# Performance work log

Measured on AMD Instinct MI355X. Metric: run time of the kernel, lower is better.

Reference implementation:

```python
import jax, jax.numpy as jnp
import numpy as np

B, L, H = 256, 16, 512
D2 = 2 * H  # bidirectional tree-LSTM hidden dim


def setup_inputs() -> dict:
    key = jax.random.key(0)
    ks = jax.random.split(key, 8)
    sc = lambda k, shp, fan: (jax.random.normal(k, shp, jnp.float32) / np.sqrt(fan)).astype(jnp.float32)
    return {
        "idiom_hidden": jax.random.normal(ks[0], (B, L, H), jnp.float32),
        "idiom_length": jax.random.randint(ks[1], (B,), 2, L + 1, jnp.int32),
        "w_ih_f": sc(ks[2], (4 * H, H), H),
        "w_hh_f": sc(ks[3], (4 * H, H), H),
        "b_f": jnp.zeros((4 * H,), jnp.float32),   # b_ih + b_hh fused
        "w_ih_b": sc(ks[4], (4 * H, H), H),
        "w_hh_b": sc(ks[5], (4 * H, H), H),
        "b_b": jnp.zeros((4 * H,), jnp.float32),
        "w_comp": sc(ks[6], (5 * D2, 2 * D2), 2 * D2),
        "b_comp": jnp.zeros((5 * D2,), jnp.float32),
        "w_query": sc(ks[7], (1, D2), D2),
    }


def _lstm(x, w_ih, w_hh, b):
    # x: (B, T, H) -> hs, cs: (B, T, H). PyTorch LSTMCell gate order: i, f, g, o.
    xg = jnp.einsum("bth,gh->btg", x, w_ih) + b  # precompute input gates

    def step(carry, xg_t):
        h, c = carry
        g = xg_t + h @ w_hh.T
        i, f, u, o = jnp.split(g, 4, axis=-1)
        c = jax.nn.sigmoid(f) * c + jax.nn.sigmoid(i) * jnp.tanh(u)
        h = jax.nn.sigmoid(o) * jnp.tanh(c)
        return (h, c), (h, c)

    z = jnp.zeros((x.shape[0], w_hh.shape[1]), x.dtype)
    _, (hs, cs) = jax.lax.scan(step, (z, z), jnp.swapaxes(xg, 0, 1))
    return jnp.swapaxes(hs, 0, 1), jnp.swapaxes(cs, 0, 1)


def _reverse_padded(x, lengths):
    # reverse first `length` positions of each sequence (batch_first)
    T = x.shape[1]
    pos = jnp.arange(T)[None, :]
    ln = lengths[:, None]
    idx = jnp.where(pos < ln, ln - 1 - pos, pos)
    return jnp.take_along_axis(x, idx[:, :, None], axis=1)


def _treelstm(hl, cl, hr, cr, w, b):
    v = jnp.concatenate([hl, hr], axis=-1) @ w.T + b
    i, fl, fr, u, o = jnp.split(v, 5, axis=-1)
    c = cl * jax.nn.sigmoid(fl + 1.0) + cr * jax.nn.sigmoid(fr + 1.0) + jnp.tanh(u) * jax.nn.sigmoid(i)
    h = jax.nn.sigmoid(o) * jnp.tanh(c)
    return h, c


def reference(idiom_hidden, idiom_length, w_ih_f, w_hh_f, b_f, w_ih_b, w_hh_b, b_b, w_comp, b_comp, w_query):
    maxd = idiom_hidden.shape[1]
    lmask = (jnp.arange(maxd)[None, :] < idiom_length[:, None]).astype(idiom_hidden.dtype)

    # bidirectional leaf LSTM
    hs_f, cs_f = _lstm(idiom_hidden, w_ih_f, w_hh_f, b_f)
    x_bw = _reverse_padded(idiom_hidden, idiom_length)
    hs_b, cs_b = _lstm(x_bw, w_ih_b, w_hh_b, b_b)
    hs_b = _reverse_padded(hs_b, idiom_length)
    cs_b = _reverse_padded(cs_b, idiom_length)
    h = jnp.concatenate([hs_f, hs_b], axis=-1)  # (B, L, 2H)
    c = jnp.concatenate([cs_f, cs_b], axis=-1)

    # iterative tree-LSTM composition (shapes shrink by 1 each step -> Python loop over depth)
    for i in range(maxd - 1):
        hl, hr = h[:, :-1, :], h[:, 1:, :]
        cl, cr = c[:, :-1, :], c[:, 1:, :]
        nh, nc = _treelstm(hl, cl, hr, cr, w_comp, b_comp)
        if i < maxd - 2:
            logits = jnp.einsum("bmd,d->bm", nh, w_query[0])
            m = lmask[:, i + 1:]
            masked = logits + (1.0 - m) * -10000.0  # eval-mode greedy_select
            sel = jax.lax.stop_gradient(
                jax.nn.one_hot(jnp.argmax(masked, axis=1), masked.shape[1], dtype=nh.dtype))
            cum = jnp.cumsum(sel, axis=1)
            left = (1.0 - cum)[:, :, None]
            right = (cum - sel)[:, :, None]
            nh = sel[:, :, None] * nh + left * hl + right * hr
            nc = sel[:, :, None] * nc + left * cl + right * cr
        done = lmask[:, i + 1][:, None, None]
        h = done * nh + (1.0 - done) * h[:, :-1, :]
        c = done * nc + (1.0 - done) * c[:, :-1, :]
    # state collapsed to a single node
    return h[:, 0, :]
```

## Files before the change

### kernel.cpp

```cpp
#include <hip/hip_runtime.h>
#include <math.h>

#define NB 256
#define LM 16
#define HID 512
#define H4 2048
#define D2 1024
#define D5 5120
#define NPAIR0 3840
#define INC_CAP 512

typedef __attribute__((ext_vector_type(8))) short bf16x8;
typedef __attribute__((ext_vector_type(4))) float f32x4;

__device__ __forceinline__ float sigm(float x) { return 1.0f / (1.0f + expf(-x)); }

__device__ __forceinline__ unsigned short bf16_rne(float f) {
    union { float f; unsigned u; } v; v.f = f;
    unsigned u = v.u;
    return (unsigned short)((u + 0x7fffu + ((u >> 16) & 1u)) >> 16);
}
__device__ __forceinline__ float bf16_tof(unsigned short h) {
    union { unsigned u; float f; } v; v.u = ((unsigned)h) << 16;
    return v.f;
}

__device__ __forceinline__ void gload16(const unsigned short* g, unsigned short* l) {
    __builtin_amdgcn_global_load_lds(
        (const __attribute__((address_space(1))) void*)(const void*)g,
        (__attribute__((address_space(3))) void*)(void*)l, 16, 0, 0);
}

__global__ __launch_bounds__(256)
void init_kernel(const int* __restrict__ lens, float* ccur,
                 unsigned short* hc_hi, unsigned short* hc_lo,
                 int* pos, int* pair, int4* rowlist0, int4* rowlist_c,
                 int* rcount, float* logits)
{
    int b = blockIdx.x, tid = threadIdx.x;
    for (int u = tid; u < HID; u += 256) {
        ccur[(size_t)b * HID + u] = 0.f;
        ccur[((size_t)NB + b) * HID + u] = 0.f;
        hc_hi[(size_t)b * HID + u] = 0;
        hc_hi[((size_t)NB + b) * HID + u] = 0;
        hc_lo[(size_t)b * HID + u] = 0;
        hc_lo[((size_t)NB + b) * HID + u] = 0;
    }
    if (tid < 16) { pos[b * 16 + tid] = tid; pair[b * 16 + tid] = tid; logits[b * 16 + tid] = -1e30f; }
    if (tid < 15) rowlist0[b * 15 + tid] = make_int4(b, tid, tid + 1, tid | (tid << 16));
    __shared__ int sbase;
    int len = lens[b];
    if (tid == 0) sbase = atomicAdd(rcount + 15, len - 1);
    __syncthreads();
    if (tid < len - 1) rowlist_c[sbase + tid] = make_int4(b, tid, tid + 1, tid | (tid << 16));
}

__global__ __launch_bounds__(256)
void split_w(const float4* __restrict__ w, unsigned short* __restrict__ hi,
             unsigned short* __restrict__ lo, int n4)
{
    for (int i = blockIdx.x * 256 + threadIdx.x; i < n4; i += gridDim.x * 256) {
        float4 f = w[i];
        ushort4 h, l;
        h.x = bf16_rne(f.x); l.x = bf16_rne(f.x - bf16_tof(h.x));
        h.y = bf16_rne(f.y); l.y = bf16_rne(f.y - bf16_tof(h.y));
        h.z = bf16_rne(f.z); l.z = bf16_rne(f.z - bf16_tof(h.z));
        h.w = bf16_rne(f.w); l.w = bf16_rne(f.w - bf16_tof(h.w));
        ((ushort4*)hi)[i] = h;
        ((ushort4*)lo)[i] = l;
    }
}

__global__ __launch_bounds__(256)
void pack_lstm_w(const float* __restrict__ w_ih_f, const float* __restrict__ w_hh_f,
                 const float* __restrict__ w_ih_b, const float* __restrict__ w_hh_b,
                 unsigned short* __restrict__ wl_hi, unsigned short* __restrict__ wl_lo)
{
    const int total4 = 2 * H4 * 256;
    for (int i = blockIdx.x * 256 + threadIdx.x; i < total4; i += gridDim.x * 256) {
        int k4 = i & 255;
        int j = (i >> 8) & 2047;
        int dir = i >> 19;
        const float* wih = dir ? w_ih_b : w_ih_f;
        const float* whh = dir ? w_hh_b : w_hh_f;
        float4 f = (k4 < 128) ? *(const float4*)(wih + (size_t)j * HID + k4 * 4)
                              : *(const float4*)(whh + (size_t)j * HID + (k4 - 128) * 4);
        ushort4 h, l;
        h.x = bf16_rne(f.x); l.x = bf16_rne(f.x - bf16_tof(h.x));
        h.y = bf16_rne(f.y); l.y = bf16_rne(f.y - bf16_tof(h.y));
        h.z = bf16_rne(f.z); l.z = bf16_rne(f.z - bf16_tof(h.z));
        h.w = bf16_rne(f.w); l.w = bf16_rne(f.w - bf16_tof(h.w));
        ((ushort4*)wl_hi)[i] = h;
        ((ushort4*)wl_lo)[i] = l;
    }
}

__global__ __launch_bounds__(256)
void gemm_lstm_g(int t, const int* __restrict__ lens,
                 const unsigned short* __restrict__ x_hi, const unsigned short* __restrict__ x_lo,
                 const unsigned short* __restrict__ hc_hi, const unsigned short* __restrict__ hc_lo,
                 const unsigned short* __restrict__ wl_hi, const unsigned short* __restrict__ wl_lo,
                 float* __restrict__ gbuf)
{
    constexpr int SA = 64 * 32;
    constexpr int SB = 128 * 32;
    constexpr int BUF = 2 * SA + 2 * SB;

    const int bid = blockIdx.x;
    const int x8 = bid & 7, r = bid >> 3;
    const int sub = r & 3, gq = r >> 2;
    const int g = x8 + 8 * gq;
    const int row0 = sub * 64;
    const int col0 = (g & 15) * 128;
    const int zz = g >> 4;
    const int dir = zz & 1;
    const int kz = zz >> 1;
    const int kbeg = kz * 512, kend = kbeg + 512;
    float* gout = gbuf + (size_t)kz * 2 * NB * H4;

    const int tid = threadIdx.x, lane = tid & 63, w = tid >> 6;
    const int wm = w >> 1, wn = w & 1;

    __shared__ __align__(16) unsigned short smem[2 * BUF];

    const int sz8 = ((lane & 3) ^ ((lane >> 3) & 3)) * 8;
    const int b0 = row0 + w * 16 + (lane >> 2);
    const int len = lens[b0];
    const int trow = dir ? ((t < len) ? (len - 1 - t) : t) : t;
    const size_t xoff = ((size_t)(b0 * LM + trow)) * HID;
    const size_t hoff = ((size_t)(dir * NB + b0)) * HID;

    size_t colOff[2];
#pragma unroll
    for (int cs = 0; cs < 2; ++cs)
        colOff[cs] = ((size_t)(dir * H4 + col0 + (w + 4 * cs) * 16 + (lane >> 2))) * 1024;

    auto stage = [&](int d, int k) {
        unsigned short* sb = smem + d * BUF;
        const unsigned short* sh = (k < HID) ? (x_hi + xoff + k) : (hc_hi + hoff + (k - HID));
        gload16(sh + sz8, sb + w * 512);
        const unsigned short* sl = (k < HID) ? (x_lo + xoff + k) : (hc_lo + hoff + (k - HID));
        gload16(sl + sz8, sb + SA + w * 512);
#pragma unroll
        for (int j = 0; j < 4; ++j) {
            const int pl = j >> 1, cs = j & 1;
            const unsigned short* wb = pl ? wl_lo : wl_hi;
            gload16(wb + colOff[cs] + k + sz8, sb + 2 * SA + pl * SB + (w + 4 * cs) * 512);
        }
    };

    f32x4 acc[2][4];
#pragma unroll
    for (int i = 0; i < 2; ++i)
#pragma unroll
        for (int j = 0; j < 4; ++j) acc[i][j] = (f32x4){0.f, 0.f, 0.f, 0.f};

    const int rsw = ((lane >> 4) ^ ((lane >> 1) & 3)) * 8;
    const int a_off = (wm * 32 + (lane & 15)) * 32 + rsw;
    const int b_off = 2 * SA + (wn * 64 + (lane & 15)) * 32 + rsw;

    stage(0, kbeg);
    __syncthreads();
    int cur = 0;
    for (int k0 = kbeg; k0 < kend; k0 += 32) {
        if (k0 + 32 < kend) stage(cur ^ 1, k0 + 32);
        const unsigned short* sb = smem + cur * BUF;
        bf16x8 ah[2], al[2];
#pragma unroll
        for (int fm = 0; fm < 2; ++fm) {
            ah[fm] = *(const bf16x8*)&sb[a_off + fm * 512];
            al[fm] = *(const bf16x8*)&sb[SA + a_off + fm * 512];
        }
#pragma unroll
        for (int fn = 0; fn < 4; ++fn) {
            bf16x8 bh = *(const bf16x8*)&sb[b_off + fn * 512];
            bf16x8 bl = *(const bf16x8*)&sb[SB + b_off + fn * 512];
#pragma unroll
            for (int fm = 0; fm < 2; ++fm) {
                acc[fm][fn] = __builtin_amdgcn_mfma_f32_16x16x32_bf16(ah[fm], bh, acc[fm][fn], 0, 0, 0);
                acc[fm][fn] = __builtin_amdgcn_mfma_f32_16x16x32_bf16(ah[fm], bl, acc[fm][fn], 0, 0, 0);
                acc[fm][fn] = __builtin_amdgcn_mfma_f32_16x16x32_bf16(al[fm], bh, acc[fm][fn], 0, 0, 0);
            }
        }
        __syncthreads();
        cur ^= 1;
    }

#pragma unroll
    for (int fm = 0; fm < 2; ++fm) {
        int rbase = row0 + wm * 32 + fm * 16 + (lane >> 4) * 4;
#pragma unroll
        for (int fn = 0; fn < 4; ++fn) {
            int c = col0 + wn * 64 + fn * 16 + (lane & 15);
#pragma unroll
            for (int q = 0; q < 4; ++q)
                gout[((size_t)(dir * NB + rbase + q)) * H4 + c] = acc[fm][fn][q];
        }
    }
}

__global__ __launch_bounds__(256)
void lstm_gate(int t, const int* __restrict__ lengths,
               const float* __restrict__ b_f, const float* __restrict__ b_b,
               const float* __restrict__ g_buf, float* __restrict__ ccur,
               unsigned short* __restrict__ hc_hi, unsigned short* __restrict__ hc_lo,
               unsigned short* __restrict__ h_hi, unsigned short* __restrict__ h_lo,
               float* __restrict__ c_seq)
{
    int b = blockIdx.x, dir = blockIdx.y, tid = threadIdx.x;
    const float* bias = dir ? b_b : b_f;
    int len = lengths[b];
    int pos = dir ? ((t < len) ? (len - 1 - t) : t) : t;
    const float* g0 = g_buf + ((size_t)(dir * NB + b)) * H4;
    const float* g1 = g0 + (size_t)2 * NB * H4;
    float* cc = ccur + ((size_t)(dir * NB + b)) * HID;
    unsigned short* hch = hc_hi + ((size_t)(dir * NB + b)) * HID;
    unsigned short* hcl = hc_lo + ((size_t)(dir * NB + b)) * HID;
    size_t so = ((size_t)(b * LM + pos)) * D2 + dir * HID;
    for (int u = tid; u < HID; u += 256) {
        float gi = g0[u]           + g1[u]           + bias[u];
        float gf = g0[HID + u]     + g1[HID + u]     + bias[HID + u];
        float gu = g0[2 * HID + u] + g1[2 * HID + u] + bias[2 * HID + u];
        float go = g0[3 * HID + u] + g1[3 * HID + u] + bias[3 * HID + u];
        float c = sigm(gf) * cc[u] + sigm(gi) * tanhf(gu);
        float h = sigm(go) * tanhf(c);
        cc[u] = c; c_seq[so + u] = c;
        unsigned short hb = bf16_rne(h);
        unsigned short hl2 = bf16_rne(h - bf16_tof(hb));
        hch[u] = hb; hcl[u] = hl2;
        h_hi[so + u] = hb; h_lo[so + u] = hl2;
    }
}

template<int BM, int KTOT, bool LOOPRT>
__global__ __launch_bounds__(256)
void gemm_pairs_g(const int4* __restrict__ rowlist, int nrows_lit,
                  const int* __restrict__ nrows_ptr, int cap,
                  const unsigned short* __restrict__ h_hi,
                  const unsigned short* __restrict__ h_lo,
                  const unsigned short* __restrict__ w_hi,
                  const unsigned short* __restrict__ w_lo,
                  float* __restrict__ vbuf)
{
    constexpr int WROWS = BM / 2;
    constexpr int FM = WROWS / 16;
    constexpr int NRS = BM / 64;
    constexpr int SA = BM * 32;
    constexpr int SB = 128 * 32;
    constexpr int BUF = 2 * SA + 2 * SB;

    int nrows = nrows_ptr ? *nrows_ptr : nrows_lit;

    int yc, kz, rt0, rtN;
    if constexpr (LOOPRT) {
        yc = blockIdx.x; kz = blockIdx.y;
        rt0 = 0; rtN = (nrows + BM - 1) / BM;
    } else {
        yc = blockIdx.y; kz = blockIdx.z;
        rt0 = blockIdx.x; rtN = rt0 + 1;
        if (rt0 * BM >= nrows) return;
    }

    const int col0 = yc * 128;
    const int kbeg = kz * KTOT;
    const int kend = kbeg + KTOT;
    float* vout = vbuf + (size_t)kz * cap * D5;

    const int tid = threadIdx.x, lane = tid & 63, w = tid >> 6;
    const int wm = w >> 1, wn = w & 1;

    __shared__ __align__(16) unsigned short smem[2 * BUF];

    const int sz8 = ((lane & 3) ^ ((lane >> 3) & 3)) * 8;
    size_t colOff[2];
#pragma unroll
    for (int cs = 0; cs < 2; ++cs)
        colOff[cs] = ((size_t)(col0 + (w + 4 * cs) * 16 + (lane >> 2))) * H4;

    const int rsw = ((lane >> 4) ^ ((lane >> 1) & 3)) * 8;
    const int a_off = (wm * WROWS + (lane & 15)) * 32 + rsw;
    const int b_off = 2 * SA + (wn * 64 + (lane & 15)) * 32 + rsw;

    for (int rt = rt0; rt < rtN; ++rt) {
        const int row0 = rt * BM;

        size_t offL[NRS], offR[NRS];
#pragma unroll
        for (int rs = 0; rs < NRS; ++rs) {
            int rr = row0 + (w + 4 * rs) * 16 + (lane >> 2);
            if (rr > nrows - 1) rr = nrows - 1;
            int4 e = rowlist[rr];
            if (e.x < 0) { e.x = 0; e.y = 0; e.z = 1; }
            offL[rs] = ((size_t)(e.x * LM + e.y)) * D2;
            offR[rs] = ((size_t)(e.x * LM + e.z)) * D2;
        }

        auto stage = [&](int d, int k) {
            unsigned short* sb = smem + d * BUF;
#pragma unroll
            for (int j = 0; j < 2 * NRS; ++j) {
                const int pl = j / NRS, rs = j % NRS;
                const int g2 = w + 4 * rs;
                const unsigned short* hb = pl ? h_lo : h_hi;
                size_t off = (k < D2) ? (offL[rs] + k) : (offR[rs] + (k - D2));
                gload16(hb + off + sz8, sb + pl * SA + g2 * 512);
            }
#pragma unroll
            for (int j = 0; j < 4; ++j) {
                const int pl = j >> 1, cs = j & 1;
                const int g2 = w + 4 * cs;
                const unsigned short* wb = pl ? w_lo : w_hi;
                gload16(wb + colOff[cs] + k + sz8, sb + 2 * SA + pl * SB + g2 * 512);
            }
        };

        f32x4 acc[FM][4];
#pragma unroll
        for (int i = 0; i < FM; ++i)
#pragma unroll
            for (int j = 0; j < 4; ++j) acc[i][j] = (f32x4){0.f, 0.f, 0.f, 0.f};

        stage(0, kbeg);
        __syncthreads();
        int cur = 0;
        for (int k0 = kbeg; k0 < kend; k0 += 32) {
            if (k0 + 32 < kend) stage(cur ^ 1, k0 + 32);
            const unsigned short* sb = smem + cur * BUF;
            bf16x8 ah[FM], al[FM];
#pragma unroll
            for (int fm = 0; fm < FM; ++fm) {
                ah[fm] = *(const bf16x8*)&sb[a_off + fm * 512];
                al[fm] = *(const bf16x8*)&sb[SA + a_off + fm * 512];
            }
#pragma unroll
            for (int fn = 0; fn < 4; ++fn) {
                bf16x8 bh = *(const bf16x8*)&sb[b_off + fn * 512];
                bf16x8 bl = *(const bf16x8*)&sb[SB + b_off + fn * 512];
#pragma unroll
                for (int fm = 0; fm < FM; ++fm) {
                    acc[fm][fn] = __builtin_amdgcn_mfma_f32_16x16x32_bf16(ah[fm], bh, acc[fm][fn], 0, 0, 0);
                    acc[fm][fn] = __builtin_amdgcn_mfma_f32_16x16x32_bf16(ah[fm], bl, acc[fm][fn], 0, 0, 0);
                    acc[fm][fn] = __builtin_amdgcn_mfma_f32_16x16x32_bf16(al[fm], bh, acc[fm][fn], 0, 0, 0);
                }
            }
            __syncthreads();
            cur ^= 1;
        }

#pragma unroll
        for (int fm = 0; fm < FM; ++fm) {
            int rbase = row0 + wm * WROWS + fm * 16 + (lane >> 4) * 4;
#pragma unroll
            for (int fn = 0; fn < 4; ++fn) {
                int c = col0 + wn * 64 + fn * 16 + (lane & 15);
#pragma unroll
                for (int q = 0; q < 4; ++q) {
                    int r2 = rbase + q;
                    if (r2 < nrows) vout[(size_t)r2 * D5 + c] = acc[fm][fn][q];
                }
            }
        }
    }
}

__device__ __forceinline__ void gates_row(int row, int4 e,
    const float* __restrict__ v_buf, int cap, int nz,
    const float* __restrict__ b_comp, const float* __restrict__ c_seq,
    const float* __restrict__ w_q,
    float* __restrict__ nh_cand, float* __restrict__ nc_cand,
    float* __restrict__ logits)
{
    int b = e.x, sL = e.y, sR = e.z;
    int cslot = e.w & 0xffff, plog = e.w >> 16;
    const float* v = v_buf + (size_t)row * D5;
    const size_t zstride = (size_t)cap * D5;
    const float* cl = c_seq + ((size_t)(b * LM + sL)) * D2;
    const float* cr = c_seq + ((size_t)(b * LM + sR)) * D2;
    float* nh = nh_cand + ((size_t)(b * 15 + cslot)) * D2;
    float* nc = nc_cand + ((size_t)(b * 15 + cslot)) * D2;

    float part = 0.f;
    for (int d = threadIdx.x; d < D2; d += 256) {
        float gi  = v[d];
        float gfl = v[D2 + d];
        float gfr = v[2 * D2 + d];
        float gu  = v[3 * D2 + d];
        float go  = v[4 * D2 + d];
        for (int z = 1; z < nz; ++z) {
            const float* vz = v + z * zstride;
            gi += vz[d]; gfl += vz[D2 + d]; gfr += vz[2 * D2 + d];
            gu += vz[3 * D2 + d]; go += vz[4 * D2 + d];
        }
        gi += b_comp[d]; gfl += b_comp[D2 + d]; gfr += b_comp[2 * D2 + d];
        gu += b_comp[3 * D2 + d]; go += b_comp[4 * D2 + d];
        float c = cl[d] * sigm(gfl + 1.0f) + cr[d] * sigm(gfr + 1.0f) + tanhf(gu) * sigm(gi);
        float h = sigm(go) * tanhf(c);
        nc[d] = c; nh[d] = h;
        part += h * w_q[d];
    }
    for (int o = 32; o > 0; o >>= 1) part += __shfl_down(part, o);
    __shared__ float wsum[4];
    if ((threadIdx.x & 63) == 0) wsum[threadIdx.x >> 6] = part;
    __syncthreads();
    if (threadIdx.x == 0) logits[b * 16 + plog] = wsum[0] + wsum[1] + wsum[2] + wsum[3];
    __syncthreads();
}

__global__ __launch_bounds__(256)
void gates_logits(const int4* __restrict__ rowlist, int nrows_lit,
                  const int* __restrict__ nrows_ptr,
                  const float* __restrict__ v_buf, int cap, int nz,
                  const float* __restrict__ b_comp,
                  const float* __restrict__ c_seq, const float* __restrict__ w_q,
                  float* __restrict__ nh, float* __restrict__ nc,
                  float* __restrict__ logits)
{
    int nrows = nrows_ptr ? *nrows_ptr : nrows_lit;
    int row = blockIdx.x;
    if (row >= nrows) return;
    int4 e = rowlist[row];
    if (e.x < 0) return;
    gates_row(row, e, v_buf, cap, nz, b_comp, c_seq, w_q, nh, nc, logits);
}

__device__ void merge_body(int iter, int b, const int* __restrict__ lengths,
                  float* __restrict__ c_seq,
                  const float* __restrict__ nh_cand, const float* __restrict__ nc_cand,
                  float* __restrict__ logits, int* __restrict__ pos_idx,
                  int* __restrict__ pair_idx, int4* __restrict__ rowlist_out,
                  int* __restrict__ rcount, int4* __restrict__ slotE,
                  int* __restrict__ slotR,
                  unsigned short* __restrict__ h_hi, unsigned short* __restrict__ h_lo)
{
    int tid = threadIdx.x;
    int M = 15 - iter;
    int len = lengths[b];
    bool act = (iter + 1) < len;

    __shared__ float sl[16];
    __shared__ int sp[16], sq[16];
    __shared__ int s_sel;

    if (tid <= M) sp[tid] = pos_idx[b * 16 + tid];
    if (tid < M) { sq[tid] = pair_idx[b * 16 + tid]; sl[tid] = logits[b * 16 + tid]; }
    __syncthreads();

    if (tid == 0) {
        int sel = -1;
        if (act) {
            float best = -INFINITY; sel = 0;
            for (int p2 = 0; p2 < M; ++p2) {
                float mv = ((iter + 1 + p2) < len) ? sl[p2] : (sl[p2] - 10000.0f);
                if (mv > best) { best = mv; sel = p2; }
            }
        }
        s_sel = sel;
    }
    __syncthreads();
    int sel = s_sel;

    if (sel >= 0) {
        int slotL = sp[sel];
        int cslot = sq[sel];
        const float* nh = nh_cand + ((size_t)(b * 15 + cslot)) * D2;
        const float* nc = nc_cand + ((size_t)(b * 15 + cslot)) * D2;
        float* cd = c_seq + ((size_t)(b * LM + slotL)) * D2;
        unsigned short* hh = h_hi + ((size_t)(b * LM + slotL)) * D2;
        unsigned short* hl = h_lo + ((size_t)(b * LM + slotL)) * D2;
        for (int d = tid; d < D2; d += 256) {
            float hv = nh[d];
            cd[d] = nc[d];
            unsigned short hb = bf16_rne(hv);
            hh[d] = hb;
            hl[d] = bf16_rne(hv - bf16_tof(hb));
        }

        if (tid == 0) {
            for (int p2 = sel + 1; p2 < M; ++p2) sp[p2] = sp[p2 + 1];
            for (int p2 = sel + 1; p2 < M - 1; ++p2) { sq[p2] = sq[p2 + 1]; sl[p2] = sl[p2 + 1]; }
            int Mn = M - 1;
            if (iter < 14) {
                int s0 = -1, s1 = -1;
                if (sel - 1 >= 0) {
                    int4 e0 = make_int4(b, sp[sel - 1], sp[sel], sq[sel - 1] | ((sel - 1) << 16));
                    s0 = atomicAdd(rcount, 1);
                    rowlist_out[s0] = e0;
                    slotE[2 * b] = e0;
                }
                if (sel <= Mn - 1) {
                    int4 e1 = make_int4(b, sp[sel], sp[sel + 1], sq[sel] | (sel << 16));
                    s1 = atomicAdd(rcount, 1);
                    rowlist_out[s1] = e1;
                    slotE[2 * b + 1] = e1;
                }
                slotR[2 * b] = s0; slotR[2 * b + 1] = s1;
            }
            for (int p2 = 0; p2 < M; ++p2) pos_idx[b * 16 + p2] = sp[p2];
            for (int p2 = 0; p2 < Mn; ++p2) { pair_idx[b * 16 + p2] = sq[p2]; logits[b * 16 + p2] = sl[p2]; }
        }
    } else {
        if (tid == 0 && iter < 14) { slotR[2 * b] = -1; slotR[2 * b + 1] = -1; }
    }
}

__global__ __launch_bounds__(256)
void merge_kernel(int iter, const int* __restrict__ lens, float* __restrict__ c_seq,
                  const float* __restrict__ nh, const float* __restrict__ nc,
                  float* __restrict__ logits, int* __restrict__ pos, int* __restrict__ pair,
                  int4* __restrict__ rowlist_out, int* __restrict__ rcount,
                  int4* __restrict__ slotE, int* __restrict__ slotR,
                  unsigned short* __restrict__ h_hi, unsigned short* __restrict__ h_lo)
{
    merge_body(iter, blockIdx.x, lens, c_seq, nh, nc, logits, pos, pair,
               rowlist_out, rcount, slotE, slotR, h_hi, h_lo);
}

__global__ __launch_bounds__(256)
void gates_merge(int it, const int* __restrict__ lens,
                 const float* __restrict__ vbuf, int cap, int nz,
                 const float* __restrict__ b_comp, float* __restrict__ c_seq,
                 const float* __restrict__ w_q,
                 float* __restrict__ nh_cand, float* __restrict__ nc_cand,
                 float* __restrict__ logits,
                 int* __restrict__ pos, int* __restrict__ pair,
                 int4* __restrict__ rowlist_out, int* __restrict__ rc_next,
                 int4* __restrict__ slotE, int* __restrict__ slotR,
                 unsigned short* __restrict__ h_hi, unsigned short* __restrict__ h_lo)
{
    int b = blockIdx.x;
    int tid = threadIdx.x;
    int slot = tid >> 7, tid2 = tid & 127;
    int row = slotR[2 * b + slot];
    int4 e = slotE[2 * b + slot];

    __shared__ float wsum2[2][2];

    float part = 0.f;
    if (row >= 0) {
        int cslot = e.w & 0xffff;
        const float* v = vbuf + (size_t)row * D5;
        const size_t zstride = (size_t)cap * D5;
        const float* cl = c_seq + ((size_t)(b * LM + e.y)) * D2;
        const float* cr = c_seq + ((size_t)(b * LM + e.z)) * D2;
        float* nh = nh_cand + ((size_t)(b * 15 + cslot)) * D2;
        float* nc = nc_cand + ((size_t)(b * 15 + cslot)) * D2;
        for (int d = tid2; d < D2; d += 128) {
            float gi  = v[d];
            float gfl = v[D2 + d];
            float gfr = v[2 * D2 + d];
            float gu  = v[3 * D2 + d];
            float go  = v[4 * D2 + d];
            for (int z = 1; z < nz; ++z) {
                const float* vz = v + z * zstride;
                gi += vz[d]; gfl += vz[D2 + d]; gfr += vz[2 * D2 + d];
                gu += vz[3 * D2 + d]; go += vz[4 * D2 + d];
            }
            gi += b_comp[d]; gfl += b_comp[D2 + d]; gfr += b_comp[2 * D2 + d];
            gu += b_comp[3 * D2 + d]; go += b_comp[4 * D2 + d];
            float c = cl[d] * sigm(gfl + 1.0f) + cr[d] * sigm(gfr + 1.0f) + tanhf(gu) * sigm(gi);
            float h = sigm(go) * tanhf(c);
            nc[d] = c; nh[d] = h;
            part += h * w_q[d];
        }
    }
    for (int o = 32; o > 0; o >>= 1) part += __shfl_down(part, o);
    if ((tid2 & 63) == 0) wsum2[slot][tid2 >> 6] = part;
    __syncthreads();
    if (row >= 0 && tid2 == 0) {
        int plog = e.w >> 16;
        logits[b * 16 + plog] = wsum2[slot][0] + wsum2[slot][1];
    }
    __syncthreads();

    merge_body(it + 1, b, lens, c_seq, nh_cand, nc_cand, logits, pos, pair,
               rowlist_out, rc_next, slotE, slotR, h_hi, h_lo);
}

__global__ __launch_bounds__(256)
void copy_out(const unsigned short* __restrict__ h_hi,
              const unsigned short* __restrict__ h_lo, float* __restrict__ out)
{
    int b = blockIdx.x;
    size_t base = (size_t)(b * LM) * D2;
    for (int d = threadIdx.x; d < D2; d += 256)
        out[(size_t)b * D2 + d] = bf16_tof(h_hi[base + d]) + bf16_tof(h_lo[base + d]);
}

extern "C" void kernel_launch(void* const* d_in, const int* in_sizes, int n_in,
                              void* d_out, int out_size, void* d_ws, size_t ws_size,
                              hipStream_t stream)
{
    const float* x      = (const float*)d_in[0];
    const int*   lens   = (const int*)  d_in[1];
    const float* w_ih_f = (const float*)d_in[2];
    const float* w_hh_f = (const float*)d_in[3];
    const float* b_f    = (const float*)d_in[4];
    const float* w_ih_b = (const float*)d_in[5];
    const float* w_hh_b = (const float*)d_in[6];
    const float* b_b    = (const float*)d_in[7];
    const float* w_comp = (const float*)d_in[8];
    const float* b_comp = (const float*)d_in[9];
    const float* w_q    = (const float*)d_in[10];
    float* out = (float*)d_out;

    char* p = (char*)d_ws;
    auto alloc = [&](size_t bytes) {
        char* q = p; p += (bytes + 255) & ~(size_t)255; return q;
    };
    float* c_seq = (float*)alloc((size_t)NB * LM * D2 * 4);
    float* nh    = (float*)alloc((size_t)NB * 15 * D2 * 4);
    float* nc    = (float*)alloc((size_t)NB * 15 * D2 * 4);
    unsigned short* h_hi = (unsigned short*)alloc((size_t)NB * LM * D2 * 2);
    unsigned short* h_lo = (unsigned short*)alloc((size_t)NB * LM * D2 * 2);
    unsigned short* w_hi = (unsigned short*)alloc((size_t)D5 * H4 * 2);
    unsigned short* w_lo = (unsigned short*)alloc((size_t)D5 * H4 * 2);
    unsigned short* x_hi = (unsigned short*)alloc((size_t)NB * LM * HID * 2);
    unsigned short* x_lo = (unsigned short*)alloc((size_t)NB * LM * HID * 2);
    unsigned short* wl_hi = (unsigned short*)alloc((size_t)2 * H4 * 1024 * 2);
    unsigned short* wl_lo = (unsigned short*)alloc((size_t)2 * H4 * 1024 * 2);
    unsigned short* hc_hi = (unsigned short*)alloc((size_t)2 * NB * HID * 2);
    unsigned short* hc_lo = (unsigned short*)alloc((size_t)2 * NB * HID * 2);
    float* ccur  = (float*)alloc((size_t)2 * NB * HID * 4);
    float* logits = (float*)alloc((size_t)NB * 16 * 4);
    int*   pos    = (int*)alloc((size_t)NB * 16 * 4);
    int*   pair   = (int*)alloc((size_t)NB * 16 * 4);
    int4*  rowlist0   = (int4*)alloc((size_t)NPAIR0 * 16);
    int4*  rowlist_c  = (int4*)alloc((size_t)NPAIR0 * 16);
    int4*  rowlist_inc= (int4*)alloc((size_t)INC_CAP * 16);
    int4*  slotE  = (int4*)alloc((size_t)2 * NB * 16);
    int*   slotR  = (int*)alloc((size_t)2 * NB * 4);
    int*   rcount = (int*)alloc(16 * 4);
    char* tail = p;
    float* gbuf = (float*)tail;
    float* vbuf = (float*)tail;

    size_t used = (size_t)(tail - (char*)d_ws);
    size_t avail = (ws_size > used) ? (ws_size - used) : 0;
    size_t maxc = avail / ((size_t)D5 * 4);
    if (maxc > (size_t)NPAIR0) maxc = NPAIR0;
    int chunk = ((int)maxc) & ~127;
    if (chunk < 2048) chunk = 2048;

    hipMemsetAsync(rcount, 0, 64, stream);
    init_kernel<<<dim3(NB), dim3(256), 0, stream>>>(lens, ccur, hc_hi, hc_lo, pos, pair,
                                                    rowlist0, rowlist_c, rcount, logits);
    split_w<<<dim3(2048), dim3(256), 0, stream>>>((const float4*)w_comp, w_hi, w_lo, (int)((size_t)D5 * H4 / 4));
    split_w<<<dim3(1024), dim3(256), 0, stream>>>((const float4*)x, x_hi, x_lo, (int)((size_t)NB * LM * HID / 4));
    pack_lstm_w<<<dim3(1024), dim3(256), 0, stream>>>(w_ih_f, w_hh_f, w_ih_b, w_hh_b, wl_hi, wl_lo);

    for (int t = 0; t < 16; ++t) {
        gemm_lstm_g<<<dim3(256), dim3(256), 0, stream>>>(
            t, lens, x_hi, x_lo, hc_hi, hc_lo, wl_hi, wl_lo, gbuf);
        lstm_gate<<<dim3(NB, 2), dim3(256), 0, stream>>>(
            t, lens, b_f, b_b, gbuf, ccur, hc_hi, hc_lo, h_hi, h_lo, c_seq);
    }

    if (chunk >= NPAIR0) {
        gemm_pairs_g<128, 2048, false><<<dim3(30, 40, 1), dim3(256), 0, stream>>>(
            rowlist_c, NPAIR0, (const int*)(rcount + 15), 0,
            h_hi, h_lo, w_hi, w_lo, vbuf);
        gates_logits<<<dim3(NPAIR0), dim3(256), 0, stream>>>(
            rowlist_c, NPAIR0, (const int*)(rcount + 15),
            vbuf, 0, 1, b_comp, c_seq, w_q, nh, nc, logits);
    } else {
        for (int off = 0; off < NPAIR0; off += chunk) {
            int rows = NPAIR0 - off; if (rows > chunk) rows = chunk;
            int RT = (rows + 127) >> 7;
            gemm_pairs_g<128, 2048, false><<<dim3(RT, 40, 1), dim3(256), 0, stream>>>(
                rowlist0 + off, rows, (const int*)nullptr, 0,
                h_hi, h_lo, w_hi, w_lo, vbuf);
            gates_logits<<<dim3(rows), dim3(256), 0, stream>>>(
                rowlist0 + off, rows, (const int*)nullptr,
                vbuf, 0, 1, b_comp, c_seq, w_q, nh, nc, logits);
        }
    }

    merge_kernel<<<dim3(NB), dim3(256), 0, stream>>>(
        0, lens, c_seq, nh, nc, logits, pos, pair,
        rowlist_inc, rcount + 0, slotE, slotR, h_hi, h_lo);
    for (int it = 0; it < 14; ++it) {
        gemm_pairs_g<128, 512, true><<<dim3(40, 4), dim3(256), 0, stream>>>(
            rowlist_inc, 0, (const int*)(rcount + it), INC_CAP,
            h_hi, h_lo, w_hi, w_lo, vbuf);
        gates_merge<<<dim3(NB), dim3(256), 0, stream>>>(
            it, lens, vbuf, INC_CAP, 4, b_comp, c_seq, w_q, nh, nc, logits,
            pos, pair, rowlist_inc, rcount + it + 1, slotE, slotR, h_hi, h_lo);
    }

    copy_out<<<dim3(NB), dim3(256), 0, stream>>>(h_hi, h_lo, out);
}
```

Measured before the change: 1.436 ms.

## Use single 512-row, 8-wave GEMM tile for incremental pair composition

The incremental tree-LSTM pair GEMM replaces the per-block loop over 128-row tiles with a new 512-thread kernel. It covers all rows up to INC_CAP in one 512x128 tile, so each weight slice is staged once per block instead of once per row tile. The old looping path is removed from the generic kernel, which now only does the single-tile case. In exchange, every block always computes 512 rows, including clamped padding rows when few pairs remain. Each wave also holds 128 accumulator floats, and the double-buffered LDS use rises to about 160 KB, which limits occupancy to one block per CU.

```diff
diff --git a/kernel.cpp b/kernel.cpp
--- a/kernel.cpp
+++ b/kernel.cpp
@@ -232,7 +232,7 @@
     }
 }
 
-template<int BM, int KTOT, bool LOOPRT>
+template<int BM, int KTOT>
 __global__ __launch_bounds__(256)
 void gemm_pairs_g(const int4* __restrict__ rowlist, int nrows_lit,
                   const int* __restrict__ nrows_ptr, int cap,
@@ -250,21 +250,12 @@
     constexpr int BUF = 2 * SA + 2 * SB;
 
     int nrows = nrows_ptr ? *nrows_ptr : nrows_lit;
-
-    int yc, kz, rt0, rtN;
-    if constexpr (LOOPRT) {
-        yc = blockIdx.x; kz = blockIdx.y;
-        rt0 = 0; rtN = (nrows + BM - 1) / BM;
-    } else {
-        yc = blockIdx.y; kz = blockIdx.z;
-        rt0 = blockIdx.x; rtN = rt0 + 1;
-        if (rt0 * BM >= nrows) return;
-    }
-
-    const int col0 = yc * 128;
-    const int kbeg = kz * KTOT;
+    const int row0 = blockIdx.x * BM;
+    if (row0 >= nrows) return;
+    const int col0 = blockIdx.y * 128;
+    const int kbeg = blockIdx.z * KTOT;
     const int kend = kbeg + KTOT;
-    float* vout = vbuf + (size_t)kz * cap * D5;
+    float* vout = vbuf + (size_t)blockIdx.z * cap * D5;
 
     const int tid = threadIdx.x, lane = tid & 63, w = tid >> 6;
     const int wm = w >> 1, wn = w & 1;
@@ -272,92 +263,193 @@
     __shared__ __align__(16) unsigned short smem[2 * BUF];
 
     const int sz8 = ((lane & 3) ^ ((lane >> 3) & 3)) * 8;
+    size_t offL[NRS], offR[NRS];
+#pragma unroll
+    for (int rs = 0; rs < NRS; ++rs) {
+        int rr = row0 + (w + 4 * rs) * 16 + (lane >> 2);
+        if (rr > nrows - 1) rr = nrows - 1;
+        int4 e = rowlist[rr];
+        if (e.x < 0) { e.x = 0; e.y = 0; e.z = 1; }
+        offL[rs] = ((size_t)(e.x * LM + e.y)) * D2;
+        offR[rs] = ((size_t)(e.x * LM + e.z)) * D2;
+    }
     size_t colOff[2];
 #pragma unroll
     for (int cs = 0; cs < 2; ++cs)
         colOff[cs] = ((size_t)(col0 + (w + 4 * cs) * 16 + (lane >> 2))) * H4;
+
+    auto stage = [&](int d, int k) {
+        unsigned short* sb = smem + d * BUF;
+#pragma unroll
+        for (int j = 0; j < 2 * NRS; ++j) {
+            const int pl = j / NRS, rs = j % NRS;
+            const int g2 = w + 4 * rs;
+            const unsigned short* hb = pl ? h_lo : h_hi;
+            size_t off = (k < D2) ? (offL[rs] + k) : (offR[rs] + (k - D2));
+            gload16(hb + off + sz8, sb + pl * SA + g2 * 512);
+        }
+#pragma unroll
+        for (int j = 0; j < 4; ++j) {
+            const int pl = j >> 1, cs = j & 1;
+            const int g2 = w + 4 * cs;
+            const unsigned short* wb = pl ? w_lo : w_hi;
+            gload16(wb + colOff[cs] + k + sz8, sb + 2 * SA + pl * SB + g2 * 512);
+        }
+    };
+
+    f32x4 acc[FM][4];
+#pragma unroll
+    for (int i = 0; i < FM; ++i)
+#pragma unroll
+        for (int j = 0; j < 4; ++j) acc[i][j] = (f32x4){0.f, 0.f, 0.f, 0.f};
 
     const int rsw = ((lane >> 4) ^ ((lane >> 1) & 3)) * 8;
     const int a_off = (wm * WROWS + (lane & 15)) * 32 + rsw;
     const int b_off = 2 * SA + (wn * 64 + (lane & 15)) * 32 + rsw;
 
-    for (int rt = rt0; rt < rtN; ++rt) {
-        const int row0 = rt * BM;
-
-        size_t offL[NRS], offR[NRS];
-#pragma unroll
-        for (int rs = 0; rs < NRS; ++rs) {
-            int rr = row0 + (w + 4 * rs) * 16 + (lane >> 2);
-            if (rr > nrows - 1) rr = nrows - 1;
-            int4 e = rowlist[rr];
-            if (e.x < 0) { e.x = 0; e.y = 0; e.z = 1; }
-            offL[rs] = ((size_t)(e.x * LM + e.y)) * D2;
-            offR[rs] = ((size_t)(e.x * LM + e.z)) * D2;
-        }
-
-        auto stage = [&](int d, int k) {
-            unsigned short* sb = smem + d * BUF;
-#pragma unroll
-            for (int j = 0; j < 2 * NRS; ++j) {
-                const int pl = j / NRS, rs = j % NRS;
-                const int g2 = w + 4 * rs;
-                const unsigned short* hb = pl ? h_lo : h_hi;
-                size_t off = (k < D2) ? (offL[rs] + k) : (offR[rs] + (k - D2));
-                gload16(hb + off + sz8, sb + pl * SA + g2 * 512);
-            }
-#pragma unroll
-            for (int j = 0; j < 4; ++j) {
-                const int pl = j >> 1, cs = j & 1;
-                const int g2 = w + 4 * cs;
-                const unsigned short* wb = pl ? w_lo : w_hi;
-                gload16(wb + colOff[cs] + k + sz8, sb + 2 * SA + pl * SB + g2 * 512);
-            }
-        };
-
-        f32x4 acc[FM][4];
-#pragma unroll
-        for (int i = 0; i < FM; ++i)
-#pragma unroll
-            for (int j = 0; j < 4; ++j) acc[i][j] = (f32x4){0.f, 0.f, 0.f, 0.f};
-
-        stage(0, kbeg);
+    stage(0, kbeg);
+    __syncthreads();
+    int cur = 0;
+    for (int k0 = kbeg; k0 < kend; k0 += 32) {
+        if (k0 + 32 < kend) stage(cur ^ 1, k0 + 32);
+        const unsigned short* sb = smem + cur * BUF;
+        bf16x8 ah[FM], al[FM];
+#pragma unroll
+        for (int fm = 0; fm < FM; ++fm) {
+            ah[fm] = *(const bf16x8*)&sb[a_off + fm * 512];
+            al[fm] = *(const bf16x8*)&sb[SA + a_off + fm * 512];
+        }
+#pragma unroll
+        for (int fn = 0; fn < 4; ++fn) {
+            bf16x8 bh = *(const bf16x8*)&sb[b_off + fn * 512];
+            bf16x8 bl = *(const bf16x8*)&sb[SB + b_off + fn * 512];
+#pragma unroll
+            for (int fm = 0; fm < FM; ++fm) {
+                acc[fm][fn] = __builtin_amdgcn_mfma_f32_16x16x32_bf16(ah[fm], bh, acc[fm][fn], 0, 0, 0);
+                acc[fm][fn] = __builtin_amdgcn_mfma_f32_16x16x32_bf16(ah[fm], bl, acc[fm][fn], 0, 0, 0);
+                acc[fm][fn] = __builtin_amdgcn_mfma_f32_16x16x32_bf16(al[fm], bh, acc[fm][fn], 0, 0, 0);
+            }
+        }
         __syncthreads();
-        int cur = 0;
-        for (int k0 = kbeg; k0 < kend; k0 += 32) {
-            if (k0 + 32 < kend) stage(cur ^ 1, k0 + 32);
-            const unsigned short* sb = smem + cur * BUF;
-            bf16x8 ah[FM], al[FM];
-#pragma unroll
-            for (int fm = 0; fm < FM; ++fm) {
-                ah[fm] = *(const bf16x8*)&sb[a_off + fm * 512];
-                al[fm] = *(const bf16x8*)&sb[SA + a_off + fm * 512];
-            }
-#pragma unroll
-            for (int fn = 0; fn < 4; ++fn) {
-                bf16x8 bh = *(const bf16x8*)&sb[b_off + fn * 512];
-                bf16x8 bl = *(const bf16x8*)&sb[SB + b_off + fn * 512];
-#pragma unroll
-                for (int fm = 0; fm < FM; ++fm) {
-                    acc[fm][fn] = __builtin_amdgcn_mfma_f32_16x16x32_bf16(ah[fm], bh, acc[fm][fn], 0, 0, 0);
-                    acc[fm][fn] = __builtin_amdgcn_mfma_f32_16x16x32_bf16(ah[fm], bl, acc[fm][fn], 0, 0, 0);
-                    acc[fm][fn] = __builtin_amdgcn_mfma_f32_16x16x32_bf16(al[fm], bh, acc[fm][fn], 0, 0, 0);
-                }
-            }
-            __syncthreads();
-            cur ^= 1;
-        }
-
-#pragma unroll
-        for (int fm = 0; fm < FM; ++fm) {
-            int rbase = row0 + wm * WROWS + fm * 16 + (lane >> 4) * 4;
-#pragma unroll
-            for (int fn = 0; fn < 4; ++fn) {
-                int c = col0 + wn * 64 + fn * 16 + (lane & 15);
-#pragma unroll
-                for (int q = 0; q < 4; ++q) {
-                    int r2 = rbase + q;
-                    if (r2 < nrows) vout[(size_t)r2 * D5 + c] = acc[fm][fn][q];
-                }
+        cur ^= 1;
+    }
+
+#pragma unroll
+    for (int fm = 0; fm < FM; ++fm) {
+        int rbase = row0 + wm * WROWS + fm * 16 + (lane >> 4) * 4;
+#pragma unroll
+        for (int fn = 0; fn < 4; ++fn) {
+            int c = col0 + wn * 64 + fn * 16 + (lane & 15);
+#pragma unroll
+            for (int q = 0; q < 4; ++q) {
+                int r2 = rbase + q;
+                if (r2 < nrows) vout[(size_t)r2 * D5 + c] = acc[fm][fn][q];
+            }
+        }
+    }
+}
+
+template<int KTOT>
+__global__ __launch_bounds__(512)
+void gemm_pairs_big(const int4* __restrict__ rowlist,
+                    const int* __restrict__ nrows_ptr, int cap,
+                    const unsigned short* __restrict__ h_hi,
+                    const unsigned short* __restrict__ h_lo,
+                    const unsigned short* __restrict__ w_hi,
+                    const unsigned short* __restrict__ w_lo,
+                    float* __restrict__ vbuf)
+{
+    constexpr int SA = 512 * 32;
+    constexpr int SB = 128 * 32;
+    constexpr int BUF = 2 * SA + 2 * SB;
+
+    int nrows = *nrows_ptr;
+    if (nrows <= 0) return;
+    const int col0 = blockIdx.x * 128;
+    const int kz = blockIdx.y;
+    const int kbeg = kz * KTOT, kend = kbeg + KTOT;
+    float* vout = vbuf + (size_t)kz * cap * D5;
+
+    const int tid = threadIdx.x, lane = tid & 63, w = tid >> 6;
+    const int wm = w >> 1, wn = w & 1;
+
+    __shared__ __align__(16) unsigned short smem[2 * BUF];
+
+    const int sz8 = ((lane & 3) ^ ((lane >> 3) & 3)) * 8;
+    size_t offL[4], offR[4];
+#pragma unroll
+    for (int i4 = 0; i4 < 4; ++i4) {
+        int rr = i4 * 128 + w * 16 + (lane >> 2);
+        if (rr > nrows - 1) rr = nrows - 1;
+        int4 e = rowlist[rr];
+        if (e.x < 0) { e.x = 0; e.y = 0; e.z = 1; }
+        offL[i4] = ((size_t)(e.x * LM + e.y)) * D2;
+        offR[i4] = ((size_t)(e.x * LM + e.z)) * D2;
+    }
+    const size_t colOff = ((size_t)(col0 + w * 16 + (lane >> 2))) * H4;
+
+    auto stage = [&](int d, int k) {
+        unsigned short* sb = smem + d * BUF;
+#pragma unroll
+        for (int pl = 0; pl < 2; ++pl) {
+            const unsigned short* hb = pl ? h_lo : h_hi;
+#pragma unroll
+            for (int i4 = 0; i4 < 4; ++i4) {
+                size_t off = (k < D2) ? (offL[i4] + k) : (offR[i4] + (k - D2));
+                gload16(hb + off + sz8, sb + pl * SA + (i4 * 128 + w * 16) * 32);
+            }
+            const unsigned short* wb = pl ? w_lo : w_hi;
+            gload16(wb + colOff + k + sz8, sb + 2 * SA + pl * SB + (w * 16) * 32);
+        }
+    };
+
+    f32x4 acc[8][4];
+#pragma unroll
+    for (int i = 0; i < 8; ++i)
+#pragma unroll
+        for (int j = 0; j < 4; ++j) acc[i][j] = (f32x4){0.f, 0.f, 0.f, 0.f};
+
+    const int rsw = ((lane >> 4) ^ ((lane >> 1) & 3)) * 8;
+    const int a_off = (wm * 128 + (lane & 15)) * 32 + rsw;
+    const int b_off = 2 * SA + (wn * 64 + (lane & 15)) * 32 + rsw;
+
+    stage(0, kbeg);
+    __syncthreads();
+    int cur = 0;
+    for (int k0 = kbeg; k0 < kend; k0 += 32) {
+        if (k0 + 32 < kend) stage(cur ^ 1, k0 + 32);
+        const unsigned short* sb = smem + cur * BUF;
+        bf16x8 ah[8], al[8];
+#pragma unroll
+        for (int fm = 0; fm < 8; ++fm) {
+            ah[fm] = *(const bf16x8*)&sb[a_off + fm * 512];
+            al[fm] = *(const bf16x8*)&sb[SA + a_off + fm * 512];
+        }
+#pragma unroll
+        for (int fn = 0; fn < 4; ++fn) {
+            bf16x8 bh = *(const bf16x8*)&sb[b_off + fn * 512];
+            bf16x8 bl = *(const bf16x8*)&sb[SB + b_off + fn * 512];
+#pragma unroll
+            for (int fm = 0; fm < 8; ++fm) {
+                acc[fm][fn] = __builtin_amdgcn_mfma_f32_16x16x32_bf16(ah[fm], bh, acc[fm][fn], 0, 0, 0);
+                acc[fm][fn] = __builtin_amdgcn_mfma_f32_16x16x32_bf16(ah[fm], bl, acc[fm][fn], 0, 0, 0);
+                acc[fm][fn] = __builtin_amdgcn_mfma_f32_16x16x32_bf16(al[fm], bh, acc[fm][fn], 0, 0, 0);
+            }
+        }
+        __syncthreads();
+        cur ^= 1;
+    }
+
+#pragma unroll
+    for (int fm = 0; fm < 8; ++fm) {
+        int rbase = wm * 128 + fm * 16 + (lane >> 4) * 4;
+#pragma unroll
+        for (int fn = 0; fn < 4; ++fn) {
+            int c = col0 + wn * 64 + fn * 16 + (lane & 15);
+#pragma unroll
+            for (int q = 0; q < 4; ++q) {
+                int r2 = rbase + q;
+                if (r2 < nrows) vout[(size_t)r2 * D5 + c] = acc[fm][fn][q];
             }
         }
     }
@@ -656,7 +748,7 @@
     }
 
     if (chunk >= NPAIR0) {
-        gemm_pairs_g<128, 2048, false><<<dim3(30, 40, 1), dim3(256), 0, stream>>>(
+        gemm_pairs_g<128, 2048><<<dim3(30, 40, 1), dim3(256), 0, stream>>>(
             rowlist_c, NPAIR0, (const int*)(rcount + 15), 0,
             h_hi, h_lo, w_hi, w_lo, vbuf);
         gates_logits<<<dim3(NPAIR0), dim3(256), 0, stream>>>(
@@ -666,7 +758,7 @@
         for (int off = 0; off < NPAIR0; off += chunk) {
             int rows = NPAIR0 - off; if (rows > chunk) rows = chunk;
             int RT = (rows + 127) >> 7;
-            gemm_pairs_g<128, 2048, false><<<dim3(RT, 40, 1), dim3(256), 0, stream>>>(
+            gemm_pairs_g<128, 2048><<<dim3(RT, 40, 1), dim3(256), 0, stream>>>(
                 rowlist0 + off, rows, (const int*)nullptr, 0,
                 h_hi, h_lo, w_hi, w_lo, vbuf);
             gates_logits<<<dim3(rows), dim3(256), 0, stream>>>(
@@ -679,8 +771,8 @@
         0, lens, c_seq, nh, nc, logits, pos, pair,
         rowlist_inc, rcount + 0, slotE, slotR, h_hi, h_lo);
     for (int it = 0; it < 14; ++it) {
-        gemm_pairs_g<128, 512, true><<<dim3(40, 4), dim3(256), 0, stream>>>(
-            rowlist_inc, 0, (const int*)(rcount + it), INC_CAP,
+        gemm_pairs_big<512><<<dim3(40, 4), dim3(512), 0, stream>>>(
+            rowlist_inc, (const int*)(rcount + it), INC_CAP,
             h_hi, h_lo, w_hi, w_lo, vbuf);
         gates_merge<<<dim3(NB), dim3(256), 0, stream>>>(
             it, lens, vbuf, INC_CAP, 4, b_comp, c_seq, w_q, nh, nc, logits,
```

Result: faster. 1.369 ms (-4.7%).
